# Performance work log

Measured on AMD Instinct MI355X. Metric: run time of the kernel, lower is better.

Reference implementation:

```python
import jax, jax.numpy as jnp
import numpy as np

B, T = 512, 300
IN_S, IN_D = 128, 64
HS, HD = 256, 128
N_NEURONS, OUT = 1000, 1


def setup_inputs() -> dict:
    key = jax.random.key(0)
    ks = jax.random.split(key, 20)
    g = lambda i, shape, s=0.05: jax.random.normal(ks[i], shape, dtype=jnp.float32) * s
    inp = {
        "x_static": jax.random.normal(ks[0], (B, IN_S), dtype=jnp.float32),
        "x_dynamic": jax.random.normal(ks[1], (B, T, IN_D), dtype=jnp.float32),
        "neuron_order": jax.random.randint(ks[2], (B,), 0, N_NEURONS, dtype=jnp.int32),
        # static MLP
        "w_s1": g(3, (HS, IN_S)), "b_s1": g(4, (HS,)),
        "w_s2": g(5, (HS, HS)), "b_s2": g(6, (HS,)),
        # dynamic projection
        "w_d": g(7, (HD, IN_D)), "b_d": g(8, (HD,)),
        # bidirectional relu-RNN (1 layer)
        "w_ih_f": g(9, (HD, HD)), "w_hh_f": g(10, (HD, HD)),
        "b_ih_f": g(11, (HD,)), "b_hh_f": g(12, (HD,)),
        "w_ih_b": g(13, (HD, HD)), "w_hh_b": g(14, (HD, HD)),
        "b_ih_b": g(15, (HD,)), "b_hh_b": g(16, (HD,)),
        # per-neuron output heads: in_dim = 2*HD + HS
        "fc_w": g(17, (N_NEURONS, OUT, 2 * HD + HS)),
        "fc_b": g(18, (N_NEURONS, OUT)),
    }
    return inp


def _rnn_dir(d, w_ih, w_hh, b_ih, b_hh, reverse):
    # d: [B, T, HD]; precompute input contribution once
    pre = d @ w_ih.T + (b_ih + b_hh)  # [B, T, HD]
    h0 = jnp.zeros((d.shape[0], w_hh.shape[0]), d.dtype)

    def step(h, x_pre):
        h = jax.nn.relu(x_pre + h @ w_hh.T)
        return h, h

    _, hs = jax.lax.scan(step, h0, jnp.swapaxes(pre, 0, 1), reverse=reverse)
    return jnp.swapaxes(hs, 0, 1)  # [B, T, HD]


def reference(x_static, x_dynamic, neuron_order,
              w_s1, b_s1, w_s2, b_s2, w_d, b_d,
              w_ih_f, w_hh_f, b_ih_f, b_hh_f,
              w_ih_b, w_hh_b, b_ih_b, b_hh_b,
              fc_w, fc_b):
    relu = jax.nn.relu
    # static MLP (dropout is identity at eval)
    s = relu(x_static @ w_s1.T + b_s1)
    s = relu(s @ w_s2.T + b_s2)  # [B, HS]
    # dynamic projection
    d = relu(x_dynamic @ w_d.T + b_d)  # [B, T, HD]
    # bidirectional relu RNN
    hf = _rnn_dir(d, w_ih_f, w_hh_f, b_ih_f, b_hh_f, reverse=False)
    hb = _rnn_dir(d, w_ih_b, w_hh_b, b_ih_b, b_hh_b, reverse=True)
    out_dyn = relu(jnp.concatenate([hf, hb], axis=-1))  # [B, T, 2*HD]
    # tile static over time and concat
    t = out_dyn.shape[1]
    final = jnp.concatenate(
        [jnp.broadcast_to(s[:, None, :], (s.shape[0], t, s.shape[1])), out_dyn],
        axis=-1)  # [B, T, HS+2*HD]
    # per-sample neuron head: gather weights then batched tiny GEMM
    Wg = fc_w[neuron_order]          # [B, OUT, HS+2*HD]
    bg = fc_b[neuron_order]          # [B, OUT]
    y = jnp.einsum('btd,bod->bto', final, Wg) + bg[:, None, :]  # [B, T, OUT]
    # torch: per-sample transpose to (OUT, T), concat over batch -> [B*OUT, T]
    out = relu(jnp.transpose(y, (0, 2, 1)).reshape(-1, t))
    return out
```

## Files before the change

kernel.cpp:

```cpp
#include <hip/hip_runtime.h>
#include <hip/hip_bf16.h>

#define BB 512
#define TT 300
#define IN_S 128
#define IN_D 64
#define HS 256
#define HD 128
#define CD 512

typedef __attribute__((ext_vector_type(8))) short bf16x8;
typedef __attribute__((ext_vector_type(4))) float f32x4;
typedef __attribute__((ext_vector_type(4))) unsigned uint4_t;
typedef unsigned short ushort_t;

static __device__ __forceinline__ ushort_t f2bf(float x) {
    unsigned u = __builtin_bit_cast(unsigned, x);
    unsigned r = (u + 0x7FFFu + ((u >> 16) & 1u)) >> 16;
    return (ushort_t)r;
}
static __device__ __forceinline__ float bflo(unsigned u) {
    return __builtin_bit_cast(float, u << 16);
}
static __device__ __forceinline__ float bfhi(unsigned u) {
    return __builtin_bit_cast(float, u & 0xffff0000u);
}
static __device__ __forceinline__ unsigned cvt_pk(float lo, float hi) {
    unsigned r;
    asm("v_cvt_pk_bf16_f32 %0, %1, %2" : "=v"(r) : "v"(lo), "v"(hi));
    return r;
}

__global__ __launch_bounds__(256) void prep_kernel(
    const float* __restrict__ wd, const float* __restrict__ wihf, const float* __restrict__ wihb,
    const float* __restrict__ whhf, const float* __restrict__ whhb,
    const float* __restrict__ bif, const float* __restrict__ bhf,
    const float* __restrict__ bib, const float* __restrict__ bhb,
    ushort_t* __restrict__ wd_bf, ushort_t* __restrict__ wihf_bf, ushort_t* __restrict__ wihb_bf,
    ushort_t* __restrict__ whhf_bf, ushort_t* __restrict__ whhb_bf,
    float* __restrict__ bsf, float* __restrict__ bsb)
{
    const int i = blockIdx.x * 256 + threadIdx.x;
    if (i < HD * IN_D) wd_bf[i] = f2bf(wd[i]);
    wihf_bf[i] = f2bf(wihf[i]);
    wihb_bf[i] = f2bf(wihb[i]);
    whhf_bf[i] = f2bf(whhf[i]);
    whhb_bf[i] = f2bf(whhb[i]);
    if (i < HD) { bsf[i] = bif[i] + bhf[i]; bsb[i] = bib[i] + bhb[i]; }
}

__global__ __launch_bounds__(256) void static_head_kernel(
    const float* __restrict__ xs, const int* __restrict__ norder,
    const float* __restrict__ w1, const float* __restrict__ b1,
    const float* __restrict__ w2, const float* __restrict__ b2,
    const float* __restrict__ fcw, const float* __restrict__ fcb,
    float* __restrict__ ds)
{
    __shared__ float xb[IN_S];
    __shared__ float s1[HS];
    __shared__ float red[4];
    const int b = blockIdx.x, tid = threadIdx.x;
    if (tid < IN_S) xb[tid] = xs[(size_t)b * IN_S + tid];
    __syncthreads();

    float a0 = 0.f, a1 = 0.f, a2 = 0.f, a3 = 0.f;
    {
        const float4* wsrc = (const float4*)(w1 + (size_t)tid * IN_S);
        const float4* x4 = (const float4*)xb;
#pragma unroll
        for (int i = 0; i < IN_S / 4; ++i) {
            float4 w = wsrc[i], x = x4[i];
            a0 = fmaf(w.x, x.x, a0); a1 = fmaf(w.y, x.y, a1);
            a2 = fmaf(w.z, x.z, a2); a3 = fmaf(w.w, x.w, a3);
        }
    }
    s1[tid] = fmaxf(b1[tid] + ((a0 + a1) + (a2 + a3)), 0.f);
    __syncthreads();

    a0 = a1 = a2 = a3 = 0.f;
    {
        const float4* wsrc = (const float4*)(w2 + (size_t)tid * HS);
        const float4* x4 = (const float4*)s1;
#pragma unroll
        for (int i = 0; i < HS / 4; ++i) {
            float4 w = wsrc[i], x = x4[i];
            a0 = fmaf(w.x, x.x, a0); a1 = fmaf(w.y, x.y, a1);
            a2 = fmaf(w.z, x.z, a2); a3 = fmaf(w.w, x.w, a3);
        }
    }
    float s2 = fmaxf(b2[tid] + ((a0 + a1) + (a2 + a3)), 0.f);

    const int n = norder[b];
    float p = s2 * fcw[(size_t)n * CD + tid];
#pragma unroll
    for (int o = 32; o >= 1; o >>= 1) p += __shfl_down(p, o);
    if ((tid & 63) == 0) red[tid >> 6] = p;
    __syncthreads();
    if (tid == 0) ds[b] = red[0] + red[1] + red[2] + red[3] + fcb[n];
}

__global__ __launch_bounds__(256) void proj_kernel(
    const float* __restrict__ xd, const ushort_t* __restrict__ wd_bf,
    const float* __restrict__ bd,
    const ushort_t* __restrict__ wihf_bf, const ushort_t* __restrict__ wihb_bf,
    const float* __restrict__ bsf, const float* __restrict__ bsb,
    ushort_t* __restrict__ preF, ushort_t* __restrict__ preB)
{
    __shared__ char lds[49152];
    char* dbase = lds;
    char* xbase = lds + 32768;
    const int tid = threadIdx.x;
    const int m0 = blockIdx.x * 128;

    {
        const int row = tid >> 1, half = tid & 1;
        const int swz = (row & 7) << 4;
        const float4* src = (const float4*)(xd + (size_t)(m0 + row) * IN_D + half * 32);
#pragma unroll
        for (int i = 0; i < 4; ++i) {
            float4 a = src[2 * i], b = src[2 * i + 1];
            const uint4_t v = {cvt_pk(a.x, a.y), cvt_pk(a.z, a.w),
                               cvt_pk(b.x, b.y), cvt_pk(b.z, b.w)};
            *(uint4_t*)(xbase + ((row * 128 + half * 64 + i * 16) ^ swz)) = v;
        }
    }
    __syncthreads();

    const int w = tid >> 6, l = tid & 63;
    const int lr = l & 15, lg = l >> 4;

    f32x4 acc[2][8];
#pragma unroll
    for (int mt = 0; mt < 2; ++mt)
#pragma unroll
        for (int nt = 0; nt < 8; ++nt) acc[mt][nt] = (f32x4){0.f, 0.f, 0.f, 0.f};

    for (int kk = 0; kk < 2; ++kk) {
        bf16x8 a[2], b[8];
#pragma unroll
        for (int mt = 0; mt < 2; ++mt) {
            const int row = (w * 2 + mt) * 16 + lr;
            a[mt] = *(const bf16x8*)(xbase + ((row * 128 + kk * 64 + lg * 16) ^ ((row & 7) << 4)));
        }
#pragma unroll
        for (int nt = 0; nt < 8; ++nt)
            b[nt] = *(const bf16x8*)(wd_bf + (nt * 16 + lr) * IN_D + kk * 32 + lg * 8);
#pragma unroll
        for (int mt = 0; mt < 2; ++mt)
#pragma unroll
            for (int nt = 0; nt < 8; ++nt)
                acc[mt][nt] = __builtin_amdgcn_mfma_f32_16x16x32_bf16(a[mt], b[nt], acc[mt][nt], 0, 0, 0);
    }
#pragma unroll
    for (int nt = 0; nt < 8; ++nt) {
        const float bj = bd[nt * 16 + lr];
        const int col2 = (nt * 16 + lr) * 2;
#pragma unroll
        for (int mt = 0; mt < 2; ++mt)
#pragma unroll
            for (int r = 0; r < 4; ++r) {
                const int row = (w * 2 + mt) * 16 + lg * 4 + r;
                const float v = fmaxf(acc[mt][nt][r] + bj, 0.f);
                *(ushort_t*)(dbase + ((row * 256 + col2) ^ ((row & 7) << 4))) = (ushort_t)cvt_pk(v, v);
            }
    }
    __syncthreads();

#pragma unroll
    for (int mat = 0; mat < 2; ++mat) {
        const ushort_t* wm = mat ? wihb_bf : wihf_bf;
        const float* bs = mat ? bsb : bsf;
        ushort_t* outp = mat ? preB : preF;

        f32x4 acc2[2][8];
#pragma unroll
        for (int mt = 0; mt < 2; ++mt)
#pragma unroll
            for (int nt = 0; nt < 8; ++nt) acc2[mt][nt] = (f32x4){0.f, 0.f, 0.f, 0.f};

        for (int kk = 0; kk < 4; ++kk) {
            bf16x8 a[2], b[8];
#pragma unroll
            for (int mt = 0; mt < 2; ++mt) {
                const int row = (w * 2 + mt) * 16 + lr;
                a[mt] = *(const bf16x8*)(dbase + ((row * 256 + kk * 64 + lg * 16) ^ ((row & 7) << 4)));
            }
#pragma unroll
            for (int nt = 0; nt < 8; ++nt)
                b[nt] = *(const bf16x8*)(wm + (nt * 16 + lr) * HD + kk * 32 + lg * 8);
#pragma unroll
            for (int mt = 0; mt < 2; ++mt)
#pragma unroll
                for (int nt = 0; nt < 8; ++nt)
                    acc2[mt][nt] = __builtin_amdgcn_mfma_f32_16x16x32_bf16(a[mt], b[nt], acc2[mt][nt], 0, 0, 0);
        }
        float bsv[8];
#pragma unroll
        for (int nt = 0; nt < 8; ++nt) bsv[nt] = bs[nt * 16 + lr];

#pragma unroll
        for (int mt = 0; mt < 2; ++mt) {
            __syncthreads();
#pragma unroll
            for (int nt = 0; nt < 8; ++nt) {
                const int col2 = (nt * 16 + lr) * 2;
#pragma unroll
                for (int r = 0; r < 4; ++r) {
                    const int rr = w * 16 + lg * 4 + r;
                    const float v = acc2[mt][nt][r] + bsv[nt];
                    *(ushort_t*)(xbase + ((rr * 256 + col2) ^ ((rr & 7) << 4))) = (ushort_t)cvt_pk(v, v);
                }
            }
            __syncthreads();
#pragma unroll
            for (int k = 0; k < 4; ++k) {
                const int seg = tid + k * 256;
                const int rr = seg >> 4, sg = seg & 15;
                const int m = m0 + (2 * (rr >> 4) + mt) * 16 + (rr & 15);
                const uint4_t val = *(const uint4_t*)(xbase + ((rr * 256 + sg * 16) ^ ((rr & 7) << 4)));
                *(uint4_t*)(outp + (size_t)m * HD + sg * 8) = val;
            }
        }
    }
}

__global__ __launch_bounds__(512, 1) void rnn_kernel(
    const ushort_t* __restrict__ preF, const ushort_t* __restrict__ preB,
    const ushort_t* __restrict__ whhF, const ushort_t* __restrict__ whhB,
    const float* __restrict__ fcw, const int* __restrict__ norder,
    float* __restrict__ dotP)
{
    __shared__ char hlds[8192];
    const int bid = blockIdx.x;
    const int dir = bid & 1;
    const int s0 = (bid >> 1) * 16;
    const ushort_t* __restrict__ pre = dir ? preB : preF;
    const ushort_t* __restrict__ whh = dir ? whhB : whhF;

    const int tid = threadIdx.x;
    const int w = tid >> 6;
    const int l = tid & 63;
    const int lr = l & 15, lg = l >> 4;

    const int jt = w;
    const int jb = (jt & 3) * 32 + lg * 8 + (jt >> 2) * 4;

    bf16x8 A[4];
#pragma unroll
    for (int kk = 0; kk < 4; ++kk) {
        const int row = (jt & 3) * 32 + (lr >> 2) * 8 + (jt >> 2) * 4 + (lr & 3);
        A[kk] = *(const bf16x8*)(whh + (size_t)row * HD + kk * 32 + lg * 8);
    }

    const int n = norder[s0 + lr];
    const float* wrow = fcw + (size_t)n * CD + HS + dir * HD;
    float wg0 = wrow[jb], wg1 = wrow[jb + 1], wg2 = wrow[jb + 2], wg3 = wrow[jb + 3];

    float* __restrict__ dotW = dotP + ((size_t)(dir * 8 + w) * TT) * BB;

    const int dt = dir ? -1 : 1;
    const int t0 = dir ? (TT - 1) : 0;
    const ushort_t* __restrict__ lane_pre = pre + (size_t)(s0 + lr) * (TT * HD) + jb;

    const int rbase = l * 16;
    const int woff = (jt & 3) * 1024 + l * 16 + (jt >> 2) * 8;

    *(uint2*)(hlds + tid * 8) = (uint2){0u, 0u};

    uint2 pA, pB, pC;
    {
        pA = *(const uint2*)(lane_pre + (size_t)t0 * HD);
        pB = *(const uint2*)(lane_pre + (size_t)(t0 + dt) * HD);
        pC = *(const uint2*)(lane_pre + (size_t)(t0 + 2 * dt) * HD);
    }
    __syncthreads();

    int t = t0;
    int cur = 0;

#define RNN_STEP(P)                                                            \
    {                                                                          \
        bf16x8 Bq[4];                                                          \
        _Pragma("unroll")                                                      \
        for (int kk = 0; kk < 4; ++kk)                                         \
            Bq[kk] = *(const bf16x8*)(hlds + cur * 4096 + kk * 1024 + rbase);  \
        f32x4 accA, accB;                                                      \
        accA[0] = bflo(P.x); accA[1] = bfhi(P.x);                              \
        accA[2] = bflo(P.y); accA[3] = bfhi(P.y);                              \
        accB = (f32x4){0.f, 0.f, 0.f, 0.f};                                    \
        {                 \
            const int tp = t + 3 * dt;                                         \
            const int tc = tp < 0 ? 0 : (tp >= TT ? TT - 1 : tp);              \
            P = *(const uint2*)(lane_pre + (size_t)tc * HD);                   \
        }                                                                      \
        accA = __builtin_amdgcn_mfma_f32_16x16x32_bf16(A[0], Bq[0], accA, 0, 0, 0); \
        accB = __builtin_amdgcn_mfma_f32_16x16x32_bf16(A[2], Bq[2], accB, 0, 0, 0); \
        accA = __builtin_amdgcn_mfma_f32_16x16x32_bf16(A[1], Bq[1], accA, 0, 0, 0); \
        accB = __builtin_amdgcn_mfma_f32_16x16x32_bf16(A[3], Bq[3], accB, 0, 0, 0); \
        const float v0 = fmaxf(accA[0] + accB[0], 0.f);                        \
        const float v1 = fmaxf(accA[1] + accB[1], 0.f);                        \
        const float v2 = fmaxf(accA[2] + accB[2], 0.f);                        \
        const float v3 = fmaxf(accA[3] + accB[3], 0.f);                        \
        const uint2 q = {cvt_pk(v0, v1), cvt_pk(v2, v3)};                      \
        *(uint2*)(hlds + (cur ^ 1) * 4096 + woff) = q;                         \
        asm volatile("s_waitcnt lgkmcnt(0)" ::: "memory");                     \
        __builtin_amdgcn_s_barrier();                                          \
           \
        float dacc = fmaf(v0, wg0, v1 * wg1) + fmaf(v2, wg2, v3 * wg3);        \
        dacc += __shfl_xor(dacc, 16);                                          \
        dacc += __shfl_xor(dacc, 32);                                          \
        if (lg == 0) dotW[(size_t)t * BB + s0 + lr] = dacc;                    \
        t += dt;                                                               \
        cur ^= 1;                                                              \
    }

    for (int it = 0; it < TT / 3; ++it) {
        RNN_STEP(pA);
        RNN_STEP(pB);
        RNN_STEP(pC);
    }
#undef RNN_STEP
}

__global__ __launch_bounds__(512) void final_kernel(
    const float* __restrict__ ds, const float* __restrict__ dotP,
    float* __restrict__ out)
{
    const int t = blockIdx.x;
    const int s = threadIdx.x;
    float acc = ds[s];
#pragma unroll
    for (int dw = 0; dw < 16; ++dw)
        acc += dotP[((size_t)dw * TT + t) * BB + s];
    out[(size_t)s * TT + t] = fmaxf(acc, 0.f);
}

extern "C" void kernel_launch(void* const* d_in, const int* in_sizes, int n_in,
                              void* d_out, int out_size, void* d_ws, size_t ws_size,
                              hipStream_t stream)
{
    const float* x_static = (const float*)d_in[0];
    const float* x_dyn    = (const float*)d_in[1];
    const int*   norder   = (const int*)d_in[2];
    const float* w_s1 = (const float*)d_in[3];  const float* b_s1 = (const float*)d_in[4];
    const float* w_s2 = (const float*)d_in[5];  const float* b_s2 = (const float*)d_in[6];
    const float* w_d  = (const float*)d_in[7];  const float* b_d  = (const float*)d_in[8];
    const float* w_ih_f = (const float*)d_in[9];  const float* w_hh_f = (const float*)d_in[10];
    const float* b_ih_f = (const float*)d_in[11]; const float* b_hh_f = (const float*)d_in[12];
    const float* w_ih_b = (const float*)d_in[13]; const float* w_hh_b = (const float*)d_in[14];
    const float* b_ih_b = (const float*)d_in[15]; const float* b_hh_b = (const float*)d_in[16];
    const float* fc_w = (const float*)d_in[17];  const float* fc_b = (const float*)d_in[18];
    float* out = (float*)d_out;

    const size_t PRE_BYTES = (size_t)BB * TT * HD * sizeof(ushort_t);
    char* p = (char*)d_ws;
    ushort_t* preF    = (ushort_t*)p;
    ushort_t* preB    = (ushort_t*)(p + PRE_BYTES);
    char* q = p + 2 * PRE_BYTES;
    ushort_t* wd_bf   = (ushort_t*)q;               q += 16384 * sizeof(ushort_t);
    ushort_t* wihf_bf = (ushort_t*)q;               q += 16384 * sizeof(ushort_t);
    ushort_t* wihb_bf = (ushort_t*)q;               q += 16384 * sizeof(ushort_t);
    ushort_t* whhf_bf = (ushort_t*)q;               q += 16384 * sizeof(ushort_t);
    ushort_t* whhb_bf = (ushort_t*)q;               q += 16384 * sizeof(ushort_t);
    float* bsf = (float*)q;                         q += 256 * sizeof(float);
    float* bsb = (float*)q;                         q += 256 * sizeof(float);
    float* ds  = (float*)q;                         q += 512 * sizeof(float);
    float* dotP = (float*)q;

    prep_kernel<<<64, 256, 0, stream>>>(w_d, w_ih_f, w_ih_b, w_hh_f, w_hh_b,
                                        b_ih_f, b_hh_f, b_ih_b, b_hh_b,
                                        wd_bf, wihf_bf, wihb_bf, whhf_bf, whhb_bf, bsf, bsb);
    static_head_kernel<<<BB, 256, 0, stream>>>(x_static, norder, w_s1, b_s1, w_s2, b_s2,
                                               fc_w, fc_b, ds);
    proj_kernel<<<(BB * TT) / 128, 256, 0, stream>>>(x_dyn, wd_bf, b_d, wihf_bf, wihb_bf,
                                                     bsf, bsb, preF, preB);
    rnn_kernel<<<64, 512, 0, stream>>>(preF, preB, whhf_bf, whhb_bf, fc_w, norder, dotP);
    final_kernel<<<TT, 512, 0, stream>>>(ds, dotP, out);
}
```

Before: 201.0 us.

## Halve proj_kernel tile to 64 rows, cache A fragments in registers, shrink LDS

The projection kernel now processes 64 rows per block instead of 128, so each wave handles one 16-row M tile. LDS drops from 48KB to 24KB, the launch bound requests 4 blocks per CU, and the grid doubles. The relu'd projection fragments are loaded once into registers and reused for both the forward and backward input GEMMs, and the output staging reuses the same LDS region with fewer barriers. In exchange, each block reloads the weight B fragments for half as many rows, which doubles global and L2 weight traffic per output.

```diff
diff --git a/kernel.cpp b/kernel.cpp
--- a/kernel.cpp
+++ b/kernel.cpp
@@ -99,71 +99,71 @@
     if (tid == 0) ds[b] = red[0] + red[1] + red[2] + red[3] + fcb[n];
 }
 
-__global__ __launch_bounds__(256) void proj_kernel(
+__global__ __launch_bounds__(256, 4) void proj_kernel(
     const float* __restrict__ xd, const ushort_t* __restrict__ wd_bf,
     const float* __restrict__ bd,
     const ushort_t* __restrict__ wihf_bf, const ushort_t* __restrict__ wihb_bf,
     const float* __restrict__ bsf, const float* __restrict__ bsb,
     ushort_t* __restrict__ preF, ushort_t* __restrict__ preB)
 {
-    __shared__ char lds[49152];
+    __shared__ char lds[24576];
     char* dbase = lds;
-    char* xbase = lds + 32768;
+    char* xbase = lds + 16384;
     const int tid = threadIdx.x;
-    const int m0 = blockIdx.x * 128;
-
-    {
-        const int row = tid >> 1, half = tid & 1;
+    const int m0 = blockIdx.x * 64;
+
+    {
+        const int row = tid >> 2, q = tid & 3;
         const int swz = (row & 7) << 4;
-        const float4* src = (const float4*)(xd + (size_t)(m0 + row) * IN_D + half * 32);
-#pragma unroll
-        for (int i = 0; i < 4; ++i) {
-            float4 a = src[2 * i], b = src[2 * i + 1];
-            const uint4_t v = {cvt_pk(a.x, a.y), cvt_pk(a.z, a.w),
-                               cvt_pk(b.x, b.y), cvt_pk(b.z, b.w)};
-            *(uint4_t*)(xbase + ((row * 128 + half * 64 + i * 16) ^ swz)) = v;
-        }
+        const float4* src = (const float4*)(xd + (size_t)(m0 + row) * IN_D + q * 16);
+        const float4 a = src[0], b = src[1], c = src[2], d = src[3];
+        const uint4_t v0 = {cvt_pk(a.x, a.y), cvt_pk(a.z, a.w),
+                            cvt_pk(b.x, b.y), cvt_pk(b.z, b.w)};
+        const uint4_t v1 = {cvt_pk(c.x, c.y), cvt_pk(c.z, c.w),
+                            cvt_pk(d.x, d.y), cvt_pk(d.z, d.w)};
+        *(uint4_t*)(xbase + ((row * 128 + q * 32) ^ swz)) = v0;
+        *(uint4_t*)(xbase + ((row * 128 + q * 32 + 16) ^ swz)) = v1;
     }
     __syncthreads();
 
     const int w = tid >> 6, l = tid & 63;
     const int lr = l & 15, lg = l >> 4;
-
-    f32x4 acc[2][8];
-#pragma unroll
-    for (int mt = 0; mt < 2; ++mt)
-#pragma unroll
-        for (int nt = 0; nt < 8; ++nt) acc[mt][nt] = (f32x4){0.f, 0.f, 0.f, 0.f};
-
-    for (int kk = 0; kk < 2; ++kk) {
-        bf16x8 a[2], b[8];
-#pragma unroll
-        for (int mt = 0; mt < 2; ++mt) {
-            const int row = (w * 2 + mt) * 16 + lr;
-            a[mt] = *(const bf16x8*)(xbase + ((row * 128 + kk * 64 + lg * 16) ^ ((row & 7) << 4)));
-        }
-#pragma unroll
-        for (int nt = 0; nt < 8; ++nt)
-            b[nt] = *(const bf16x8*)(wd_bf + (nt * 16 + lr) * IN_D + kk * 32 + lg * 8);
-#pragma unroll
-        for (int mt = 0; mt < 2; ++mt)
+    const int arow = w * 16 + lr;
+    const int aswz = (arow & 7) << 4;
+
+    {
+        f32x4 acc1[8];
+#pragma unroll
+        for (int nt = 0; nt < 8; ++nt) acc1[nt] = (f32x4){0.f, 0.f, 0.f, 0.f};
+#pragma unroll
+        for (int kk = 0; kk < 2; ++kk) {
+            const bf16x8 a1 = *(const bf16x8*)(xbase + ((arow * 128 + kk * 64 + lg * 16) ^ aswz));
+            bf16x8 b[8];
 #pragma unroll
             for (int nt = 0; nt < 8; ++nt)
-                acc[mt][nt] = __builtin_amdgcn_mfma_f32_16x16x32_bf16(a[mt], b[nt], acc[mt][nt], 0, 0, 0);
-    }
-#pragma unroll
-    for (int nt = 0; nt < 8; ++nt) {
-        const float bj = bd[nt * 16 + lr];
-        const int col2 = (nt * 16 + lr) * 2;
-#pragma unroll
-        for (int mt = 0; mt < 2; ++mt)
+                b[nt] = *(const bf16x8*)(wd_bf + (size_t)(nt * 16 + lr) * IN_D + kk * 32 + lg * 8);
+#pragma unroll
+            for (int nt = 0; nt < 8; ++nt)
+                acc1[nt] = __builtin_amdgcn_mfma_f32_16x16x32_bf16(a1, b[nt], acc1[nt], 0, 0, 0);
+        }
+#pragma unroll
+        for (int nt = 0; nt < 8; ++nt) {
+            const float bj = bd[nt * 16 + lr];
+            const int col2 = (nt * 16 + lr) * 2;
 #pragma unroll
             for (int r = 0; r < 4; ++r) {
-                const int row = (w * 2 + mt) * 16 + lg * 4 + r;
-                const float v = fmaxf(acc[mt][nt][r] + bj, 0.f);
+                const int row = w * 16 + lg * 4 + r;
+                const float v = fmaxf(acc1[nt][r] + bj, 0.f);
                 *(ushort_t*)(dbase + ((row * 256 + col2) ^ ((row & 7) << 4))) = (ushort_t)cvt_pk(v, v);
             }
-    }
+        }
+    }
+    __syncthreads();
+
+    bf16x8 Bd[4];
+#pragma unroll
+    for (int kk = 0; kk < 4; ++kk)
+        Bd[kk] = *(const bf16x8*)(dbase + ((arow * 256 + kk * 64 + lg * 16) ^ aswz));
     __syncthreads();
 
 #pragma unroll
@@ -172,55 +172,40 @@
         const float* bs = mat ? bsb : bsf;
         ushort_t* outp = mat ? preB : preF;
 
-        f32x4 acc2[2][8];
-#pragma unroll
-        for (int mt = 0; mt < 2; ++mt)
-#pragma unroll
-            for (int nt = 0; nt < 8; ++nt) acc2[mt][nt] = (f32x4){0.f, 0.f, 0.f, 0.f};
-
+        f32x4 acc2[8];
+#pragma unroll
+        for (int nt = 0; nt < 8; ++nt) acc2[nt] = (f32x4){0.f, 0.f, 0.f, 0.f};
+#pragma unroll
         for (int kk = 0; kk < 4; ++kk) {
-            bf16x8 a[2], b[8];
-#pragma unroll
-            for (int mt = 0; mt < 2; ++mt) {
-                const int row = (w * 2 + mt) * 16 + lr;
-                a[mt] = *(const bf16x8*)(dbase + ((row * 256 + kk * 64 + lg * 16) ^ ((row & 7) << 4)));
+            bf16x8 b[8];
+#pragma unroll
+            for (int nt = 0; nt < 8; ++nt)
+                b[nt] = *(const bf16x8*)(wm + (size_t)(nt * 16 + lr) * HD + kk * 32 + lg * 8);
+#pragma unroll
+            for (int nt = 0; nt < 8; ++nt)
+                acc2[nt] = __builtin_amdgcn_mfma_f32_16x16x32_bf16(Bd[kk], b[nt], acc2[nt], 0, 0, 0);
+        }
+
+#pragma unroll
+        for (int nt = 0; nt < 8; ++nt) {
+            const float bj = bs[nt * 16 + lr];
+            const int col2 = (nt * 16 + lr) * 2;
+#pragma unroll
+            for (int r = 0; r < 4; ++r) {
+                const int rr = w * 16 + lg * 4 + r;
+                const float v = acc2[nt][r] + bj;
+                *(ushort_t*)(dbase + ((rr * 256 + col2) ^ ((rr & 7) << 4))) = (ushort_t)cvt_pk(v, v);
             }
-#pragma unroll
-            for (int nt = 0; nt < 8; ++nt)
-                b[nt] = *(const bf16x8*)(wm + (nt * 16 + lr) * HD + kk * 32 + lg * 8);
-#pragma unroll
-            for (int mt = 0; mt < 2; ++mt)
-#pragma unroll
-                for (int nt = 0; nt < 8; ++nt)
-                    acc2[mt][nt] = __builtin_amdgcn_mfma_f32_16x16x32_bf16(a[mt], b[nt], acc2[mt][nt], 0, 0, 0);
-        }
-        float bsv[8];
-#pragma unroll
-        for (int nt = 0; nt < 8; ++nt) bsv[nt] = bs[nt * 16 + lr];
-
-#pragma unroll
-        for (int mt = 0; mt < 2; ++mt) {
-            __syncthreads();
-#pragma unroll
-            for (int nt = 0; nt < 8; ++nt) {
-                const int col2 = (nt * 16 + lr) * 2;
-#pragma unroll
-                for (int r = 0; r < 4; ++r) {
-                    const int rr = w * 16 + lg * 4 + r;
-                    const float v = acc2[mt][nt][r] + bsv[nt];
-                    *(ushort_t*)(xbase + ((rr * 256 + col2) ^ ((rr & 7) << 4))) = (ushort_t)cvt_pk(v, v);
-                }
-            }
-            __syncthreads();
-#pragma unroll
-            for (int k = 0; k < 4; ++k) {
-                const int seg = tid + k * 256;
-                const int rr = seg >> 4, sg = seg & 15;
-                const int m = m0 + (2 * (rr >> 4) + mt) * 16 + (rr & 15);
-                const uint4_t val = *(const uint4_t*)(xbase + ((rr * 256 + sg * 16) ^ ((rr & 7) << 4)));
-                *(uint4_t*)(outp + (size_t)m * HD + sg * 8) = val;
-            }
-        }
+        }
+        __syncthreads();
+#pragma unroll
+        for (int k = 0; k < 4; ++k) {
+            const int seg = tid + k * 256;
+            const int rr = seg >> 4, sg = seg & 15;
+            const uint4_t val = *(const uint4_t*)(dbase + ((rr * 256 + sg * 16) ^ ((rr & 7) << 4)));
+            *(uint4_t*)(outp + (size_t)(m0 + rr) * HD + sg * 8) = val;
+        }
+        if (mat == 0) __syncthreads();
     }
 }
 
@@ -372,8 +357,8 @@
                                         wd_bf, wihf_bf, wihb_bf, whhf_bf, whhb_bf, bsf, bsb);
     static_head_kernel<<<BB, 256, 0, stream>>>(x_static, norder, w_s1, b_s1, w_s2, b_s2,
                                                fc_w, fc_b, ds);
-    proj_kernel<<<(BB * TT) / 128, 256, 0, stream>>>(x_dyn, wd_bf, b_d, wihf_bf, wihb_bf,
-                                                     bsf, bsb, preF, preB);
+    proj_kernel<<<(BB * TT) / 64, 256, 0, stream>>>(x_dyn, wd_bf, b_d, wihf_bf, wihb_bf,
+                                                    bsf, bsb, preF, preB);
     rnn_kernel<<<64, 512, 0, stream>>>(preF, preB, whhf_bf, whhb_bf, fc_w, norder, dotP);
     final_kernel<<<TT, 512, 0, stream>>>(ds, dotP, out);
 }
```

New measurement: 245.2 us. 22.0% more time.
